# Kernel optimization log

Measured on AMD Instinct MI355X. Metric: run time of the kernel, lower is better.

## Reference

```python
import jax, jax.numpy as jnp
import numpy as np
import math

EMBED_DIM = 1024
NUM_HEADS = 16
HEAD_DIM = EMBED_DIM // NUM_HEADS
WINDOW_SIZE = 32  # one-sided; full window = 2*w+1 = 65
SCALING = math.sqrt(HEAD_DIM)


def setup_inputs() -> dict:
    key = jax.random.key(0)
    ks = jax.random.split(key, 9)
    B, S, E = 2, 2048, EMBED_DIM
    s = 1.0 / math.sqrt(E)
    inp = {
        "hidden_states": jax.random.normal(ks[0], (B, S, E), dtype=jnp.float32),
        "q_w": jax.random.uniform(ks[1], (E, E), jnp.float32, -s, s),
        "q_b": jax.random.uniform(ks[2], (E,), jnp.float32, -s, s),
        "k_w": jax.random.uniform(ks[3], (E, E), jnp.float32, -s, s),
        "k_b": jax.random.uniform(ks[4], (E,), jnp.float32, -s, s),
        "v_w": jax.random.uniform(ks[5], (E, E), jnp.float32, -s, s),
        "v_b": jax.random.uniform(ks[6], (E,), jnp.float32, -s, s),
        "o_w": jax.random.uniform(ks[7], (E, E), jnp.float32, -s, s),
        "o_b": jax.random.uniform(ks[8], (E,), jnp.float32, -s, s),
    }
    return inp


def reference(hidden_states, q_w, q_b, k_w, k_b, v_w, v_b, o_w, o_b):
    B, S, E = hidden_states.shape
    H, D, w = NUM_HEADS, HEAD_DIM, WINDOW_SIZE
    W = 2 * w + 1

    q = hidden_states @ q_w.T + q_b
    k = hidden_states @ k_w.T + k_b
    v = hidden_states @ v_w.T + v_b

    # [B, H, S, D]
    q = q.reshape(B, S, H, D).transpose(0, 2, 1, 3)
    k = k.reshape(B, S, H, D).transpose(0, 2, 1, 3)
    v = v.reshape(B, S, H, D).transpose(0, 2, 1, 3)

    # zero-pad seq dim by w on each side (matches F.pad value=0); padded keys
    # contribute score 0 (NOT -inf) exactly like the original unfold scheme.
    k_pad = jnp.pad(k, ((0, 0), (0, 0), (w, w), (0, 0)))
    v_pad = jnp.pad(v, ((0, 0), (0, 0), (w, w), (0, 0)))

    # window gather indices: query i sees padded positions i..i+2w (orig i-w..i+w)
    idx = jnp.arange(S)[:, None] + jnp.arange(W)[None, :]  # [S, W]
    k_slice = k_pad[:, :, idx]  # [B, H, S, W, D]
    v_slice = v_pad[:, :, idx]  # [B, H, S, W, D]

    score = jnp.einsum('bhsd,bhswd->bhsw', q, k_slice) / SCALING
    p = jax.nn.softmax(score, axis=-1)
    attn = jnp.einsum('bhsw,bhswd->bhsd', p, v_slice)

    attn = attn.transpose(0, 2, 1, 3).reshape(B, S, E)
    return attn @ o_w.T + o_b
```

## Files before the change

### kernel.cpp

```cpp
#include <hip/hip_runtime.h>
#include <math.h>

typedef _Float16 h16;
typedef _Float16 h8 __attribute__((ext_vector_type(8)));
typedef float f32x4 __attribute__((ext_vector_type(4)));

__device__ inline void gl2lds16(const void* g, void* l) {
  __builtin_amdgcn_global_load_lds(
      (const __attribute__((address_space(1))) void*)g,
      (__attribute__((address_space(3))) void*)l, 16, 0, 0);
}

__device__ inline void barrier_raw() {
  asm volatile("" ::: "memory");
  __builtin_amdgcn_s_barrier();
  asm volatile("" ::: "memory");
}

#define VMCNT(N) asm volatile("s_waitcnt vmcnt(" #N ")" ::: "memory")

__global__ __launch_bounds__(256) void f2h_all(
    const float* __restrict__ hs, const float* __restrict__ w0,
    const float* __restrict__ w1, const float* __restrict__ w2,
    const float* __restrict__ w3, h16* __restrict__ dst, int hsN) {
  int i = (blockIdx.x * 256 + threadIdx.x) * 8;
  const int tot = hsN + 4 * 1048576;
  if (i >= tot) return;
  const float* src;
  int off;
  if (i < hsN) {
    src = hs; off = i;
  } else {
    int k = i - hsN;
    int seg = k >> 20;
    off = k & 1048575;
    src = seg == 0 ? w0 : seg == 1 ? w1 : seg == 2 ? w2 : w3;
  }
  float4 a = *(const float4*)(src + off);
  float4 b = *(const float4*)(src + off + 4);
  h8 o;
  o[0] = (h16)a.x; o[1] = (h16)a.y; o[2] = (h16)a.z; o[3] = (h16)a.w;
  o[4] = (h16)b.x; o[5] = (h16)b.y; o[6] = (h16)b.z; o[7] = (h16)b.w;
  *(h8*)(dst + i) = o;
}

__global__ __launch_bounds__(256) void qkv97(
    const h16* __restrict__ A, const h16* __restrict__ Bw,
    const float* __restrict__ qb, const float* __restrict__ kb,
    const float* __restrict__ vb, h16* __restrict__ qo, h16* __restrict__ ko,
    h16* __restrict__ vo) {
  __shared__ __align__(16) h16 Ash[128 * 32];
  __shared__ __align__(16) h16 Bsh[128 * 32];
  __shared__ __align__(16) h16 Csh[128 * 136];

  const int tid = threadIdx.x;
  const int wid = tid >> 6, lane = tid & 63;
  const int lr = lane & 15, lg = lane >> 4;
  const int wr = wid >> 1, wc = wid & 1;
  const int srow = tid >> 2;
  const int csw = ((tid & 3) ^ ((srow >> 1) & 3)) * 8;

  const int xcd = blockIdx.x & 7;
  const int i = blockIdx.x >> 3;
  const int ibm = i & 7, ibn = i >> 3;
  const int bm = (xcd & 3) * 8 + ibm;
  const int bn = (xcd >> 2) * 12 + ibn;
  const int row0 = bm * 128, col0 = bn * 128;

  const h16* Ag = A + (size_t)row0 * 1024;
  const h16* Bg = Bw + (size_t)col0 * 1024;

  auto ldf = [&](const h16* base, int row) -> h8 {
    return *(const h8*)(base + row * 32 + (lg ^ ((row >> 1) & 3)) * 8);
  };

  f32x4 acc[4][4] = {};

  for (int t = 0; t < 32; ++t) {
    const int kof = t * 32 + csw;
    gl2lds16(Ag + (size_t)srow * 1024 + kof, &Ash[(wid * 16) * 32]);
    gl2lds16(Ag + (size_t)(64 + srow) * 1024 + kof, &Ash[(64 + wid * 16) * 32]);
    gl2lds16(Bg + (size_t)srow * 1024 + kof, &Bsh[(wid * 16) * 32]);
    gl2lds16(Bg + (size_t)(64 + srow) * 1024 + kof, &Bsh[(64 + wid * 16) * 32]);
    __syncthreads();
    h8 af[4], bf[4];
#pragma unroll
    for (int m = 0; m < 4; ++m) af[m] = ldf(Ash, wr * 64 + m * 16 + lr);
#pragma unroll
    for (int n = 0; n < 4; ++n) bf[n] = ldf(Bsh, wc * 64 + n * 16 + lr);
    __builtin_amdgcn_s_setprio(1);
#pragma unroll
    for (int m = 0; m < 4; ++m)
#pragma unroll
      for (int n = 0; n < 4; ++n)
        acc[m][n] =
            __builtin_amdgcn_mfma_f32_16x16x32_f16(af[m], bf[n], acc[m][n], 0, 0, 0);
    __builtin_amdgcn_s_setprio(0);
    __syncthreads();
  }

  const int tsel = bn >> 3;
  const int colseg = (bn & 7) * 128;
  const float* bp = tsel == 0 ? qb : (tsel == 1 ? kb : vb);
  h16* outp = tsel == 0 ? qo : (tsel == 1 ? ko : vo);

#pragma unroll
  for (int n = 0; n < 4; ++n) {
    const int ccol = wc * 64 + n * 16 + lr;
    const float bv = bp[colseg + ccol];
#pragma unroll
    for (int m = 0; m < 4; ++m)
#pragma unroll
      for (int j = 0; j < 4; ++j)
        Csh[(wr * 64 + m * 16 + lg * 4 + j) * 136 + ccol] =
            (h16)(acc[m][n][j] + bv);
  }
  __syncthreads();
#pragma unroll
  for (int p = 0; p < 8; ++p) {
    const int idx = p * 256 + tid;
    const int r = idx >> 4, c = idx & 15;
    h8 v = *(const h8*)&Csh[r * 136 + c * 8];
    *(h8*)&outp[(size_t)(row0 + r) * 1024 + colseg + c * 8] = v;
  }
}

__global__ __launch_bounds__(256) void oproj9(const h16* __restrict__ A,
                                              const h16* __restrict__ Bw,
                                              const float* __restrict__ b0,
                                              float* __restrict__ Cf) {
  __shared__ __align__(16) h16 Abuf[2][64][32];
  __shared__ __align__(16) h16 Bbuf[2][128][32];

  const int tid = threadIdx.x;
  const int wid = tid >> 6, lane = tid & 63;
  const int lr = lane & 15, lg = lane >> 4;
  const int wr = wid >> 1, wc = wid & 1;
  const int srow = tid >> 2;
  const int csw = ((tid & 3) ^ ((srow >> 1) & 3)) * 8;

  const int xcd = blockIdx.x & 7;
  const int i = blockIdx.x >> 3;
  const int bm = xcd * 8 + (i & 7);
  const int bn = i >> 3;
  const int row0 = bm * 64, col0 = bn * 128;

  const h16* Ag = A + (size_t)row0 * 1024;
  const h16* Bg = Bw + (size_t)col0 * 1024;

  auto stage = [&](int t, int bi) {
    const int kof = t * 32 + csw;
    gl2lds16(Ag + (size_t)srow * 1024 + kof, &Abuf[bi][wid * 16][0]);
    gl2lds16(Bg + (size_t)srow * 1024 + kof, &Bbuf[bi][wid * 16][0]);
    gl2lds16(Bg + (size_t)(64 + srow) * 1024 + kof, &Bbuf[bi][64 + wid * 16][0]);
  };
  auto ldf = [&](const h16* base, int row) -> h8 {
    return *(const h8*)(base + row * 32 + (lg ^ ((row >> 1) & 3)) * 8);
  };

  f32x4 acc[2][4] = {};

  stage(0, 0);
  for (int t = 0; t < 32; ++t) {
    if (t < 31) {
      stage(t + 1, (t + 1) & 1);
      VMCNT(3);
    } else {
      VMCNT(0);
    }
    barrier_raw();
    const h16* Ar = &Abuf[t & 1][0][0];
    const h16* Br = &Bbuf[t & 1][0][0];
    h8 af[2], bf[4];
#pragma unroll
    for (int m = 0; m < 2; ++m) af[m] = ldf(Ar, wr * 32 + m * 16 + lr);
#pragma unroll
    for (int n = 0; n < 4; ++n) bf[n] = ldf(Br, wc * 64 + n * 16 + lr);
    __builtin_amdgcn_s_setprio(1);
#pragma unroll
    for (int m = 0; m < 2; ++m)
#pragma unroll
      for (int n = 0; n < 4; ++n)
        acc[m][n] =
            __builtin_amdgcn_mfma_f32_16x16x32_f16(af[m], bf[n], acc[m][n], 0, 0, 0);
    __builtin_amdgcn_s_setprio(0);
    barrier_raw();
  }

#pragma unroll
  for (int n = 0; n < 4; ++n) {
    const int cidx = col0 + wc * 64 + n * 16 + lr;
    const float bv = b0[cidx];
#pragma unroll
    for (int m = 0; m < 2; ++m)
#pragma unroll
      for (int j = 0; j < 4; ++j) {
        const int r = row0 + wr * 32 + m * 16 + lg * 4 + j;
        Cf[(size_t)r * 1024 + cidx] = acc[m][n][j] + bv;
      }
  }
}

__global__ __launch_bounds__(256) void swattn(const h16* __restrict__ Q,
                                              const h16* __restrict__ K,
                                              const h16* __restrict__ V,
                                              h16* __restrict__ O) {
  __shared__ __align__(16) h16 Ksh[128 * 72];
  __shared__ __align__(16) h16 Vsh[64 * 136];
  __shared__ __align__(16) h16 Psh[4][16 * 136];

  const int qb0 = blockIdx.x * 64;
  const int bh = blockIdx.y;
  const int b = bh >> 4, h = bh & 15;
  const int tid = threadIdx.x;
  const int wave = tid >> 6, lane = tid & 63;
  const int lr = lane & 15, lg = lane >> 4;

  const h16* Qb = Q + (size_t)b * 2048 * 1024 + h * 64;
  const h16* Kb = K + (size_t)b * 2048 * 1024 + h * 64;
  const h16* Vb = V + (size_t)b * 2048 * 1024 + h * 64;

#pragma unroll
  for (int i = 0; i < 4; ++i) {
    const int c = tid * 4 + i;
    const int row = c >> 3, c8 = c & 7;
    const int t = qb0 - 32 + row;
    h8 kv, vv;
    if (t >= 0 && t < 2048) {
      kv = *(const h8*)&Kb[(size_t)t * 1024 + c8 * 8];
      vv = *(const h8*)&Vb[(size_t)t * 1024 + c8 * 8];
    } else {
#pragma unroll
      for (int j = 0; j < 8; ++j) { kv[j] = (h16)0.f; vv[j] = (h16)0.f; }
    }
    *(h8*)&Ksh[row * 72 + c8 * 8] = kv;
#pragma unroll
    for (int j = 0; j < 8; ++j) Vsh[(c8 * 8 + j) * 136 + row] = vv[j];
  }
  __syncthreads();

  const int qrow = qb0 + wave * 16 + lr;
  h8 qa[2];
#pragma unroll
  for (int kk = 0; kk < 2; ++kk)
    qa[kk] = *(const h8*)&Qb[(size_t)qrow * 1024 + kk * 32 + lg * 8];

  f32x4 sacc[8] = {};
#pragma unroll
  for (int n = 0; n < 8; ++n)
#pragma unroll
    for (int kk = 0; kk < 2; ++kk) {
      h8 kb = *(const h8*)&Ksh[(n * 16 + lr) * 72 + kk * 32 + lg * 8];
      sacc[n] = __builtin_amdgcn_mfma_f32_16x16x32_f16(qa[kk], kb, sacc[n], 0, 0, 0);
    }

  float p[8][4];
#pragma unroll
  for (int j = 0; j < 4; ++j) {
    const int wrow = wave * 16 + lg * 4 + j;
    float mx = -1e30f;
#pragma unroll
    for (int n = 0; n < 8; ++n) {
      const int d = n * 16 + lr - wrow;
      float s = (d < 0 || d > 64) ? -1e30f : sacc[n][j] * 0.125f;
      p[n][j] = s;
      mx = fmaxf(mx, s);
    }
#pragma unroll
    for (int off = 1; off < 16; off <<= 1) mx = fmaxf(mx, __shfl_xor(mx, off, 64));
    float sum = 0.f;
#pragma unroll
    for (int n = 0; n < 8; ++n) {
      const float e = __expf(p[n][j] - mx);
      p[n][j] = e;
      sum += e;
    }
#pragma unroll
    for (int off = 1; off < 16; off <<= 1) sum += __shfl_xor(sum, off, 64);
    const float inv = 1.f / sum;
#pragma unroll
    for (int n = 0; n < 8; ++n) p[n][j] *= inv;
  }

#pragma unroll
  for (int n = 0; n < 8; ++n)
#pragma unroll
    for (int j = 0; j < 4; ++j)
      Psh[wave][(lg * 4 + j) * 136 + n * 16 + lr] = (h16)p[n][j];
  __syncthreads();

  f32x4 oacc[4] = {};
#pragma unroll
  for (int kk = 0; kk < 4; ++kk) {
    h8 pa = *(const h8*)&Psh[wave][lr * 136 + kk * 32 + lg * 8];
#pragma unroll
    for (int n = 0; n < 4; ++n) {
      h8 vb = *(const h8*)&Vsh[(n * 16 + lr) * 136 + kk * 32 + lg * 8];
      oacc[n] = __builtin_amdgcn_mfma_f32_16x16x32_f16(pa, vb, oacc[n], 0, 0, 0);
    }
  }

#pragma unroll
  for (int n = 0; n < 4; ++n)
#pragma unroll
    for (int j = 0; j < 4; ++j) {
      const int s = qb0 + wave * 16 + lg * 4 + j;
      const int d = n * 16 + lr;
      O[((size_t)b * 2048 + s) * 1024 + h * 64 + d] = (h16)oacc[n][j];
    }
}

extern "C" void kernel_launch(void* const* d_in, const int* in_sizes, int n_in,
                              void* d_out, int out_size, void* d_ws, size_t ws_size,
                              hipStream_t stream) {
  const float* hs = (const float*)d_in[0];
  const float* qw = (const float*)d_in[1];
  const float* qb = (const float*)d_in[2];
  const float* kw = (const float*)d_in[3];
  const float* kb = (const float*)d_in[4];
  const float* vw = (const float*)d_in[5];
  const float* vb = (const float*)d_in[6];
  const float* ow = (const float*)d_in[7];
  const float* ob = (const float*)d_in[8];

  const int M = in_sizes[0] / 1024;

  h16* hsH = (h16*)d_ws;
  h16* wqkv = hsH + (size_t)M * 1024;
  h16* woH = wqkv + (size_t)3072 * 1024;
  h16* qH = woH + (size_t)1024 * 1024;
  h16* kH = qH + (size_t)M * 1024;
  h16* vH = kH + (size_t)M * 1024;
  h16* attnH = vH + (size_t)M * 1024;

  const int tot = M * 1024 + 4 * 1048576;
  f2h_all<<<(tot / 8 + 255) / 256, 256, 0, stream>>>(hs, qw, kw, vw, ow, hsH,
                                                     M * 1024);

  qkv97<<<768, 256, 0, stream>>>(hsH, wqkv, qb, kb, vb, qH, kH, vH);

  swattn<<<dim3(32, M / 2048 * 16), 256, 0, stream>>>(qH, kH, vH, attnH);

  oproj9<<<512, 256, 0, stream>>>(attnH, woH, ob, (float*)d_out);
}
```

Measured before the change: 86.89 us.

## Halve GEMM N-tile to 64, double grid, add per-wave epilogue staging

The QKV and output-projection GEMMs now use 64-wide column tiles instead of 128, which doubles the block count (1536 and 1024) and sets launch bounds to 6 blocks per CU. The QKV epilogue swaps the large shared-memory C tile for a small per-wave staging buffer, which cuts LDS use. The aim is better occupancy and CU fill on the 256-CU part. The cost is lower arithmetic intensity per block, since A tiles are reloaded twice as often, and fewer MFMAs per barrier.

```diff
diff --git a/kernel.cpp b/kernel.cpp
--- a/kernel.cpp
+++ b/kernel.cpp
@@ -18,6 +18,7 @@
 }
 
 #define VMCNT(N) asm volatile("s_waitcnt vmcnt(" #N ")" ::: "memory")
+#define LGKM(N) asm volatile("s_waitcnt lgkmcnt(" #N ")" ::: "memory")
 
 __global__ __launch_bounds__(256) void f2h_all(
     const float* __restrict__ hs, const float* __restrict__ w0,
@@ -44,14 +45,14 @@
   *(h8*)(dst + i) = o;
 }
 
-__global__ __launch_bounds__(256) void qkv97(
+__global__ __launch_bounds__(256, 6) void qkv10(
     const h16* __restrict__ A, const h16* __restrict__ Bw,
     const float* __restrict__ qb, const float* __restrict__ kb,
     const float* __restrict__ vb, h16* __restrict__ qo, h16* __restrict__ ko,
     h16* __restrict__ vo) {
   __shared__ __align__(16) h16 Ash[128 * 32];
-  __shared__ __align__(16) h16 Bsh[128 * 32];
-  __shared__ __align__(16) h16 Csh[128 * 136];
+  __shared__ __align__(16) h16 Bsh[64 * 32];
+  __shared__ __align__(16) h16 Cw[4][16 * 40];
 
   const int tid = threadIdx.x;
   const int wid = tid >> 6, lane = tid & 63;
@@ -62,75 +63,75 @@
 
   const int xcd = blockIdx.x & 7;
   const int i = blockIdx.x >> 3;
-  const int ibm = i & 7, ibn = i >> 3;
-  const int bm = (xcd & 3) * 8 + ibm;
-  const int bn = (xcd >> 2) * 12 + ibn;
-  const int row0 = bm * 128, col0 = bn * 128;
+  const int bm = (xcd & 3) * 8 + (i & 7);
+  const int bn = (xcd >> 2) * 24 + (i >> 3);
+  const int row0 = bm * 128, col0s = bn * 64;
 
   const h16* Ag = A + (size_t)row0 * 1024;
-  const h16* Bg = Bw + (size_t)col0 * 1024;
+  const h16* Bg = Bw + (size_t)bn * 64 * 1024;
 
   auto ldf = [&](const h16* base, int row) -> h8 {
     return *(const h8*)(base + row * 32 + (lg ^ ((row >> 1) & 3)) * 8);
   };
 
-  f32x4 acc[4][4] = {};
+  f32x4 acc[4][2] = {};
 
   for (int t = 0; t < 32; ++t) {
     const int kof = t * 32 + csw;
     gl2lds16(Ag + (size_t)srow * 1024 + kof, &Ash[(wid * 16) * 32]);
     gl2lds16(Ag + (size_t)(64 + srow) * 1024 + kof, &Ash[(64 + wid * 16) * 32]);
     gl2lds16(Bg + (size_t)srow * 1024 + kof, &Bsh[(wid * 16) * 32]);
-    gl2lds16(Bg + (size_t)(64 + srow) * 1024 + kof, &Bsh[(64 + wid * 16) * 32]);
     __syncthreads();
-    h8 af[4], bf[4];
+    h8 af[4], bf[2];
 #pragma unroll
     for (int m = 0; m < 4; ++m) af[m] = ldf(Ash, wr * 64 + m * 16 + lr);
 #pragma unroll
-    for (int n = 0; n < 4; ++n) bf[n] = ldf(Bsh, wc * 64 + n * 16 + lr);
+    for (int n = 0; n < 2; ++n) bf[n] = ldf(Bsh, wc * 32 + n * 16 + lr);
     __builtin_amdgcn_s_setprio(1);
 #pragma unroll
     for (int m = 0; m < 4; ++m)
 #pragma unroll
-      for (int n = 0; n < 4; ++n)
+      for (int n = 0; n < 2; ++n)
         acc[m][n] =
             __builtin_amdgcn_mfma_f32_16x16x32_f16(af[m], bf[n], acc[m][n], 0, 0, 0);
     __builtin_amdgcn_s_setprio(0);
     __syncthreads();
   }
 
-  const int tsel = bn >> 3;
-  const int colseg = (bn & 7) * 128;
+  const int tsel = bn >> 4;
+  const int colseg = (bn & 15) * 64;
   const float* bp = tsel == 0 ? qb : (tsel == 1 ? kb : vb);
   h16* outp = tsel == 0 ? qo : (tsel == 1 ? ko : vo);
 
-#pragma unroll
-  for (int n = 0; n < 4; ++n) {
-    const int ccol = wc * 64 + n * 16 + lr;
-    const float bv = bp[colseg + ccol];
-#pragma unroll
-    for (int m = 0; m < 4; ++m)
-#pragma unroll
-      for (int j = 0; j < 4; ++j)
-        Csh[(wr * 64 + m * 16 + lg * 4 + j) * 136 + ccol] =
-            (h16)(acc[m][n][j] + bv);
-  }
-  __syncthreads();
-#pragma unroll
-  for (int p = 0; p < 8; ++p) {
-    const int idx = p * 256 + tid;
-    const int r = idx >> 4, c = idx & 15;
-    h8 v = *(const h8*)&Csh[r * 136 + c * 8];
-    *(h8*)&outp[(size_t)(row0 + r) * 1024 + colseg + c * 8] = v;
-  }
-}
-
-__global__ __launch_bounds__(256) void oproj9(const h16* __restrict__ A,
-                                              const h16* __restrict__ Bw,
-                                              const float* __restrict__ b0,
-                                              float* __restrict__ Cf) {
+  const float bv0 = bp[colseg + wc * 32 + 0 * 16 + lr];
+  const float bv1 = bp[colseg + wc * 32 + 1 * 16 + lr];
+
+  const int erow = lane >> 2;
+  const int eslot = lane & 3;
+
+#pragma unroll
+  for (int m = 0; m < 4; ++m) {
+#pragma unroll
+    for (int j = 0; j < 4; ++j) {
+      Cw[wid][(lg * 4 + j) * 40 + 0 * 16 + lr] = (h16)(acc[m][0][j] + bv0);
+      Cw[wid][(lg * 4 + j) * 40 + 1 * 16 + lr] = (h16)(acc[m][1][j] + bv1);
+    }
+    LGKM(0);
+    __builtin_amdgcn_sched_barrier(0);
+    h8 v = *(const h8*)&Cw[wid][erow * 40 + eslot * 8];
+    const int r = row0 + wr * 64 + m * 16 + erow;
+    *(h8*)&outp[(size_t)r * 1024 + colseg + wc * 32 + eslot * 8] = v;
+    LGKM(0);
+    __builtin_amdgcn_sched_barrier(0);
+  }
+}
+
+__global__ __launch_bounds__(256, 6) void oproj10(const h16* __restrict__ A,
+                                                  const h16* __restrict__ Bw,
+                                                  const float* __restrict__ b0,
+                                                  float* __restrict__ Cf) {
   __shared__ __align__(16) h16 Abuf[2][64][32];
-  __shared__ __align__(16) h16 Bbuf[2][128][32];
+  __shared__ __align__(16) h16 Bbuf[2][64][32];
 
   const int tid = threadIdx.x;
   const int wid = tid >> 6, lane = tid & 63;
@@ -143,7 +144,7 @@
   const int i = blockIdx.x >> 3;
   const int bm = xcd * 8 + (i & 7);
   const int bn = i >> 3;
-  const int row0 = bm * 64, col0 = bn * 128;
+  const int row0 = bm * 64, col0 = bn * 64;
 
   const h16* Ag = A + (size_t)row0 * 1024;
   const h16* Bg = Bw + (size_t)col0 * 1024;
@@ -152,35 +153,34 @@
     const int kof = t * 32 + csw;
     gl2lds16(Ag + (size_t)srow * 1024 + kof, &Abuf[bi][wid * 16][0]);
     gl2lds16(Bg + (size_t)srow * 1024 + kof, &Bbuf[bi][wid * 16][0]);
-    gl2lds16(Bg + (size_t)(64 + srow) * 1024 + kof, &Bbuf[bi][64 + wid * 16][0]);
   };
   auto ldf = [&](const h16* base, int row) -> h8 {
     return *(const h8*)(base + row * 32 + (lg ^ ((row >> 1) & 3)) * 8);
   };
 
-  f32x4 acc[2][4] = {};
+  f32x4 acc[2][2] = {};
 
   stage(0, 0);
   for (int t = 0; t < 32; ++t) {
     if (t < 31) {
       stage(t + 1, (t + 1) & 1);
-      VMCNT(3);
+      VMCNT(2);
     } else {
       VMCNT(0);
     }
     barrier_raw();
     const h16* Ar = &Abuf[t & 1][0][0];
     const h16* Br = &Bbuf[t & 1][0][0];
-    h8 af[2], bf[4];
+    h8 af[2], bf[2];
 #pragma unroll
     for (int m = 0; m < 2; ++m) af[m] = ldf(Ar, wr * 32 + m * 16 + lr);
 #pragma unroll
-    for (int n = 0; n < 4; ++n) bf[n] = ldf(Br, wc * 64 + n * 16 + lr);
+    for (int n = 0; n < 2; ++n) bf[n] = ldf(Br, wc * 32 + n * 16 + lr);
     __builtin_amdgcn_s_setprio(1);
 #pragma unroll
     for (int m = 0; m < 2; ++m)
 #pragma unroll
-      for (int n = 0; n < 4; ++n)
+      for (int n = 0; n < 2; ++n)
         acc[m][n] =
             __builtin_amdgcn_mfma_f32_16x16x32_f16(af[m], bf[n], acc[m][n], 0, 0, 0);
     __builtin_amdgcn_s_setprio(0);
@@ -188,8 +188,8 @@
   }
 
 #pragma unroll
-  for (int n = 0; n < 4; ++n) {
-    const int cidx = col0 + wc * 64 + n * 16 + lr;
+  for (int n = 0; n < 2; ++n) {
+    const int cidx = col0 + wc * 32 + n * 16 + lr;
     const float bv = b0[cidx];
 #pragma unroll
     for (int m = 0; m < 2; ++m)
@@ -337,9 +337,9 @@
   f2h_all<<<(tot / 8 + 255) / 256, 256, 0, stream>>>(hs, qw, kw, vw, ow, hsH,
                                                      M * 1024);
 
-  qkv97<<<768, 256, 0, stream>>>(hsH, wqkv, qb, kb, vb, qH, kH, vH);
+  qkv10<<<1536, 256, 0, stream>>>(hsH, wqkv, qb, kb, vb, qH, kH, vH);
 
   swattn<<<dim3(32, M / 2048 * 16), 256, 0, stream>>>(qH, kH, vH, attnH);
 
-  oproj9<<<512, 256, 0, stream>>>(attnH, woH, ob, (float*)d_out);
-}
+  oproj10<<<1024, 256, 0, stream>>>(attnH, woH, ob, (float*)d_out);
+}
```

New measurement: 88.60 us. About the same (+2.0%).

## Fuse hidden-state fp16 conversion into QKV GEMM and shrink o-proj tile

Applied to the files above, without the earlier changes.

The QKV GEMM now reads fp32 hidden states directly, converting them to fp16 in registers and writing them to LDS with a register prefetch of the next K-slice. This removes the separate hidden-state conversion pass and its workspace round trip, so the conversion kernel now handles only the weights. Separately, the output projection uses 64x64 tiles with twice as many blocks and an occupancy hint, which raises parallelism but reuses each loaded tile less. The A-operand load in QKV now goes through VGPRs instead of direct global-to-LDS loads, which adds register pressure.

```diff
diff --git a/kernel.cpp b/kernel.cpp
--- a/kernel.cpp
+++ b/kernel.cpp
@@ -19,23 +19,14 @@
 
 #define VMCNT(N) asm volatile("s_waitcnt vmcnt(" #N ")" ::: "memory")
 
-__global__ __launch_bounds__(256) void f2h_all(
-    const float* __restrict__ hs, const float* __restrict__ w0,
-    const float* __restrict__ w1, const float* __restrict__ w2,
-    const float* __restrict__ w3, h16* __restrict__ dst, int hsN) {
+__global__ __launch_bounds__(256) void f2h_w(
+    const float* __restrict__ w0, const float* __restrict__ w1,
+    const float* __restrict__ w2, const float* __restrict__ w3,
+    h16* __restrict__ dst) {
   int i = (blockIdx.x * 256 + threadIdx.x) * 8;
-  const int tot = hsN + 4 * 1048576;
-  if (i >= tot) return;
-  const float* src;
-  int off;
-  if (i < hsN) {
-    src = hs; off = i;
-  } else {
-    int k = i - hsN;
-    int seg = k >> 20;
-    off = k & 1048575;
-    src = seg == 0 ? w0 : seg == 1 ? w1 : seg == 2 ? w2 : w3;
-  }
+  const int seg = i >> 20;
+  const int off = i & 1048575;
+  const float* src = seg == 0 ? w0 : seg == 1 ? w1 : seg == 2 ? w2 : w3;
   float4 a = *(const float4*)(src + off);
   float4 b = *(const float4*)(src + off + 4);
   h8 o;
@@ -44,8 +35,8 @@
   *(h8*)(dst + i) = o;
 }
 
-__global__ __launch_bounds__(256) void qkv97(
-    const h16* __restrict__ A, const h16* __restrict__ Bw,
+__global__ __launch_bounds__(256) void qkv12(
+    const float* __restrict__ A32, const h16* __restrict__ Bw,
     const float* __restrict__ qb, const float* __restrict__ kb,
     const float* __restrict__ vb, h16* __restrict__ qo, h16* __restrict__ ko,
     h16* __restrict__ vo) {
@@ -62,26 +53,51 @@
 
   const int xcd = blockIdx.x & 7;
   const int i = blockIdx.x >> 3;
-  const int ibm = i & 7, ibn = i >> 3;
-  const int bm = (xcd & 3) * 8 + ibm;
-  const int bn = (xcd >> 2) * 12 + ibn;
+  const int bm = (xcd & 3) * 8 + (i & 7);
+  const int bn = (xcd >> 2) * 12 + (i >> 3);
   const int row0 = bm * 128, col0 = bn * 128;
 
-  const h16* Ag = A + (size_t)row0 * 1024;
+  const float* Ag = A32 + (size_t)row0 * 1024;
   const h16* Bg = Bw + (size_t)col0 * 1024;
 
+  const int arow = tid >> 1;
+  const int acol = (tid & 1) * 16;
+  const int aswz = (arow >> 1) & 3;
+  const int aslot0 = (tid & 1) * 2;
+  const float* Asrc = Ag + (size_t)arow * 1024 + acol;
+
+  float4 ar[4];
+  auto loadA = [&](int t) {
+    const float* s = Asrc + t * 32;
+#pragma unroll
+    for (int l = 0; l < 4; ++l) ar[l] = *(const float4*)(s + l * 4);
+  };
+  auto writeA = [&]() {
+    h8 o0, o1;
+    o0[0] = (h16)ar[0].x; o0[1] = (h16)ar[0].y;
+    o0[2] = (h16)ar[0].z; o0[3] = (h16)ar[0].w;
+    o0[4] = (h16)ar[1].x; o0[5] = (h16)ar[1].y;
+    o0[6] = (h16)ar[1].z; o0[7] = (h16)ar[1].w;
+    o1[0] = (h16)ar[2].x; o1[1] = (h16)ar[2].y;
+    o1[2] = (h16)ar[2].z; o1[3] = (h16)ar[2].w;
+    o1[4] = (h16)ar[3].x; o1[5] = (h16)ar[3].y;
+    o1[6] = (h16)ar[3].z; o1[7] = (h16)ar[3].w;
+    *(h8*)&Ash[arow * 32 + ((aslot0) ^ aswz) * 8] = o0;
+    *(h8*)&Ash[arow * 32 + ((aslot0 + 1) ^ aswz) * 8] = o1;
+  };
   auto ldf = [&](const h16* base, int row) -> h8 {
     return *(const h8*)(base + row * 32 + (lg ^ ((row >> 1) & 3)) * 8);
   };
 
   f32x4 acc[4][4] = {};
 
+  loadA(0);
   for (int t = 0; t < 32; ++t) {
     const int kof = t * 32 + csw;
-    gl2lds16(Ag + (size_t)srow * 1024 + kof, &Ash[(wid * 16) * 32]);
-    gl2lds16(Ag + (size_t)(64 + srow) * 1024 + kof, &Ash[(64 + wid * 16) * 32]);
     gl2lds16(Bg + (size_t)srow * 1024 + kof, &Bsh[(wid * 16) * 32]);
     gl2lds16(Bg + (size_t)(64 + srow) * 1024 + kof, &Bsh[(64 + wid * 16) * 32]);
+    writeA();
+    if (t + 1 < 32) loadA(t + 1);
     __syncthreads();
     h8 af[4], bf[4];
 #pragma unroll
@@ -125,12 +141,12 @@
   }
 }
 
-__global__ __launch_bounds__(256) void oproj9(const h16* __restrict__ A,
-                                              const h16* __restrict__ Bw,
-                                              const float* __restrict__ b0,
-                                              float* __restrict__ Cf) {
+__global__ __launch_bounds__(256, 6) void oproj10(const h16* __restrict__ A,
+                                                  const h16* __restrict__ Bw,
+                                                  const float* __restrict__ b0,
+                                                  float* __restrict__ Cf) {
   __shared__ __align__(16) h16 Abuf[2][64][32];
-  __shared__ __align__(16) h16 Bbuf[2][128][32];
+  __shared__ __align__(16) h16 Bbuf[2][64][32];
 
   const int tid = threadIdx.x;
   const int wid = tid >> 6, lane = tid & 63;
@@ -143,7 +159,7 @@
   const int i = blockIdx.x >> 3;
   const int bm = xcd * 8 + (i & 7);
   const int bn = i >> 3;
-  const int row0 = bm * 64, col0 = bn * 128;
+  const int row0 = bm * 64, col0 = bn * 64;
 
   const h16* Ag = A + (size_t)row0 * 1024;
   const h16* Bg = Bw + (size_t)col0 * 1024;
@@ -152,35 +168,34 @@
     const int kof = t * 32 + csw;
     gl2lds16(Ag + (size_t)srow * 1024 + kof, &Abuf[bi][wid * 16][0]);
     gl2lds16(Bg + (size_t)srow * 1024 + kof, &Bbuf[bi][wid * 16][0]);
-    gl2lds16(Bg + (size_t)(64 + srow) * 1024 + kof, &Bbuf[bi][64 + wid * 16][0]);
   };
   auto ldf = [&](const h16* base, int row) -> h8 {
     return *(const h8*)(base + row * 32 + (lg ^ ((row >> 1) & 3)) * 8);
   };
 
-  f32x4 acc[2][4] = {};
+  f32x4 acc[2][2] = {};
 
   stage(0, 0);
   for (int t = 0; t < 32; ++t) {
     if (t < 31) {
       stage(t + 1, (t + 1) & 1);
-      VMCNT(3);
+      VMCNT(2);
     } else {
       VMCNT(0);
     }
     barrier_raw();
     const h16* Ar = &Abuf[t & 1][0][0];
     const h16* Br = &Bbuf[t & 1][0][0];
-    h8 af[2], bf[4];
+    h8 af[2], bf[2];
 #pragma unroll
     for (int m = 0; m < 2; ++m) af[m] = ldf(Ar, wr * 32 + m * 16 + lr);
 #pragma unroll
-    for (int n = 0; n < 4; ++n) bf[n] = ldf(Br, wc * 64 + n * 16 + lr);
+    for (int n = 0; n < 2; ++n) bf[n] = ldf(Br, wc * 32 + n * 16 + lr);
     __builtin_amdgcn_s_setprio(1);
 #pragma unroll
     for (int m = 0; m < 2; ++m)
 #pragma unroll
-      for (int n = 0; n < 4; ++n)
+      for (int n = 0; n < 2; ++n)
         acc[m][n] =
             __builtin_amdgcn_mfma_f32_16x16x32_f16(af[m], bf[n], acc[m][n], 0, 0, 0);
     __builtin_amdgcn_s_setprio(0);
@@ -188,8 +203,8 @@
   }
 
 #pragma unroll
-  for (int n = 0; n < 4; ++n) {
-    const int cidx = col0 + wc * 64 + n * 16 + lr;
+  for (int n = 0; n < 2; ++n) {
+    const int cidx = col0 + wc * 32 + n * 16 + lr;
     const float bv = b0[cidx];
 #pragma unroll
     for (int m = 0; m < 2; ++m)
@@ -325,21 +340,18 @@
 
   const int M = in_sizes[0] / 1024;
 
-  h16* hsH = (h16*)d_ws;
-  h16* wqkv = hsH + (size_t)M * 1024;
+  h16* wqkv = (h16*)d_ws;
   h16* woH = wqkv + (size_t)3072 * 1024;
   h16* qH = woH + (size_t)1024 * 1024;
   h16* kH = qH + (size_t)M * 1024;
   h16* vH = kH + (size_t)M * 1024;
   h16* attnH = vH + (size_t)M * 1024;
 
-  const int tot = M * 1024 + 4 * 1048576;
-  f2h_all<<<(tot / 8 + 255) / 256, 256, 0, stream>>>(hs, qw, kw, vw, ow, hsH,
-                                                     M * 1024);
-
-  qkv97<<<768, 256, 0, stream>>>(hsH, wqkv, qb, kb, vb, qH, kH, vH);
+  f2h_w<<<2048, 256, 0, stream>>>(qw, kw, vw, ow, wqkv);
+
+  qkv12<<<768, 256, 0, stream>>>(hs, wqkv, qb, kb, vb, qH, kH, vH);
 
   swattn<<<dim3(32, M / 2048 * 16), 256, 0, stream>>>(qH, kH, vH, attnH);
 
-  oproj9<<<512, 256, 0, stream>>>(attnH, woH, ob, (float*)d_out);
-}
+  oproj10<<<1024, 256, 0, stream>>>(attnH, woH, ob, (float*)d_out);
+}
```

Measured after the change: 109.8 us. 1.26x slower.
